# Optimization experiments

Measured on AMD Instinct MI355X. Metric: run time of the kernel, lower is better.

The kernel has to match this reference:

```python
import jax, jax.numpy as jnp
import numpy as np

TAU = 0.7        # init kwarg tau
BIG_NEG = -1.0e9 # matches torch big_neg
B, R = 8192, 4096


def setup_inputs() -> dict:
    key = jax.random.key(0)
    k1, k2 = jax.random.split(key)
    s = jax.random.normal(k1, (B, R), dtype=jnp.float32)
    mask = jax.random.uniform(k2, (B, R), dtype=jnp.float32)  # compared against 0.5
    return {"s": s, "mask": mask, "k": 8}


def reference(s, mask, k):
    # mask-apply then temperature scale
    z = jnp.where(mask > 0.5, s, jnp.full_like(s, BIG_NEG)) / max(TAU, 1e-6)
    # sparsemax along axis 1: sort descending, cumsum, support-size threshold
    z_sorted = -jnp.sort(-z, axis=1)                       # [B, R] descending
    z_cumsum = jnp.cumsum(z_sorted, axis=1)                # [B, R]
    r = jnp.arange(1, R + 1, dtype=z.dtype)[None, :]       # [1, R] ranks 1..R
    cond = 1.0 + r * z_sorted > z_cumsum                   # [B, R] support indicator
    k_sup = jnp.sum(cond, axis=1, keepdims=True)           # [B, 1] int support size
    tau_star = (jnp.take_along_axis(z_cumsum, k_sup - 1, axis=1) - 1.0) / k_sup.astype(z.dtype)
    p = jnp.maximum(z - tau_star, 0.0)                     # sparsemax probs, sum=1
    # scale by budget k and clip to [0, 1]
    return jnp.minimum(jnp.asarray(float(k), z.dtype) * p, 1.0)
```

## Files before the change

kernel.cpp:

```cpp
#include <hip/hip_runtime.h>


#define R_DIM 4096
#define BLOCK 256
#define V4T   4
#define BIG_NEG -1.0e9f
#define INV_TAU (1.0f / 0.7f)

__global__ __launch_bounds__(BLOCK, 6)
void gate_sparsemax_k_kernel(const float* __restrict__ s,
                             const float* __restrict__ m,
                             const int*  __restrict__ kptr,
                             float* __restrict__ out)
{
    __shared__ float red_sum[4];
    __shared__ float red_cnt[4];
    __shared__ float red_max[4];

    const int tid  = (int)threadIdx.x;
    const int lane = tid & 63;
    const int wid  = tid >> 6;
    const int row  = (int)blockIdx.x;

    const float kf = (float)(*kptr);

    const size_t base = (size_t)row * R_DIM;
    const float4* sv4 = (const float4*)(s + base);
    const float4* mv4 = (const float4*)(m + base);
    float4*       ov4 = (float4*)(out + base);

    float4 sv[V4T], mv[V4T];
    #pragma unroll
    for (int t = 0; t < V4T; ++t) sv[t] = sv4[t * BLOCK + tid];
    #pragma unroll
    for (int t = 0; t < V4T; ++t) mv[t] = mv4[t * BLOCK + tid];

    float4 zz[V4T];
    float zmax = -3.4028235e38f;
    #pragma unroll
    for (int t = 0; t < V4T; ++t) {
        float4 zv;
        zv.x = (mv[t].x > 0.5f ? sv[t].x : BIG_NEG) * INV_TAU;
        zv.y = (mv[t].y > 0.5f ? sv[t].y : BIG_NEG) * INV_TAU;
        zv.z = (mv[t].z > 0.5f ? sv[t].z : BIG_NEG) * INV_TAU;
        zv.w = (mv[t].w > 0.5f ? sv[t].w : BIG_NEG) * INV_TAU;
        zz[t] = zv;
        zmax = fmaxf(zmax, fmaxf(fmaxf(zv.x, zv.y), fmaxf(zv.z, zv.w)));
    }

    #pragma unroll
    for (int off = 32; off >= 1; off >>= 1)
        zmax = fmaxf(zmax, __shfl_xor(zmax, off, 64));
    if (lane == 0) red_max[wid] = zmax;
    __syncthreads();
    zmax = fmaxf(fmaxf(red_max[0], red_max[1]), fmaxf(red_max[2], red_max[3]));

    float tau = zmax - 1.0f;
    for (int it = 0; it < 50; ++it) {
        float ssum = 0.0f, cnt = 0.0f;
        #pragma unroll
        for (int t = 0; t < V4T; ++t) {
            const float4 zv = zz[t];
            if (zv.x > tau) { ssum += zv.x; cnt += 1.0f; }
            if (zv.y > tau) { ssum += zv.y; cnt += 1.0f; }
            if (zv.z > tau) { ssum += zv.z; cnt += 1.0f; }
            if (zv.w > tau) { ssum += zv.w; cnt += 1.0f; }
        }
        #pragma unroll
        for (int off = 32; off >= 1; off >>= 1) {
            ssum += __shfl_xor(ssum, off, 64);
            cnt  += __shfl_xor(cnt,  off, 64);
        }
        __syncthreads();
        if (lane == 0) { red_sum[wid] = ssum; red_cnt[wid] = cnt; }
        __syncthreads();
        const float S = ((red_sum[0] + red_sum[1]) + (red_sum[2] + red_sum[3]));
        const float C = ((red_cnt[0] + red_cnt[1]) + (red_cnt[2] + red_cnt[3]));
        const float tnew = (S - 1.0f) / C;
        if (tnew == tau) break;
        tau = tnew;
    }

    #pragma unroll
    for (int t = 0; t < V4T; ++t) {
        const float4 zv = zz[t];
        float4 ov;
        ov.x = fminf(kf * fmaxf(zv.x - tau, 0.0f), 1.0f);
        ov.y = fminf(kf * fmaxf(zv.y - tau, 0.0f), 1.0f);
        ov.z = fminf(kf * fmaxf(zv.z - tau, 0.0f), 1.0f);
        ov.w = fminf(kf * fmaxf(zv.w - tau, 0.0f), 1.0f);
        ov4[t * BLOCK + tid] = ov;
    }
}

extern "C" void kernel_launch(void* const* d_in, const int* in_sizes, int n_in,
                              void* d_out, int out_size, void* d_ws, size_t ws_size,
                              hipStream_t stream) {
    const float* s = (const float*)d_in[0];
    const float* m = (const float*)d_in[1];
    const int*   k = (const int*)d_in[2];
    float* out = (float*)d_out;

    const int nrows = in_sizes[0] / R_DIM;
    gate_sparsemax_k_kernel<<<nrows, BLOCK, 0, stream>>>(s, m, k, out);
}
```

Measured before the change: 312.4 us.

## Use nontemporal loads/stores, double-buffer reduction slots, relax launch bounds

Loads and stores now go through nontemporal builtins so streaming data does not pollute the cache. A scheduling barrier after the loads keeps them issued together. The per-iteration reduction uses ping-pong shared slots, which drops one of the two __syncthreads per bisection iteration. Launch bounds drop from 6 to 4 blocks per CU, which may change register allocation and occupancy.

```diff
diff --git a/kernel.cpp b/kernel.cpp
--- a/kernel.cpp
+++ b/kernel.cpp
@@ -7,14 +7,16 @@
 #define BIG_NEG -1.0e9f
 #define INV_TAU (1.0f / 0.7f)
 
-__global__ __launch_bounds__(BLOCK, 6)
+typedef float fx4 __attribute__((ext_vector_type(4)));
+
+__global__ __launch_bounds__(BLOCK, 4)
 void gate_sparsemax_k_kernel(const float* __restrict__ s,
                              const float* __restrict__ m,
                              const int*  __restrict__ kptr,
                              float* __restrict__ out)
 {
-    __shared__ float red_sum[4];
-    __shared__ float red_cnt[4];
+    __shared__ float red_sum[2][4];
+    __shared__ float red_cnt[2][4];
     __shared__ float red_max[4];
 
     const int tid  = (int)threadIdx.x;
@@ -25,21 +27,22 @@
     const float kf = (float)(*kptr);
 
     const size_t base = (size_t)row * R_DIM;
-    const float4* sv4 = (const float4*)(s + base);
-    const float4* mv4 = (const float4*)(m + base);
-    float4*       ov4 = (float4*)(out + base);
+    const fx4* sv4 = (const fx4*)(s + base);
+    const fx4* mv4 = (const fx4*)(m + base);
+    fx4*       ov4 = (fx4*)(out + base);
 
-    float4 sv[V4T], mv[V4T];
+    fx4 sv[V4T], mv[V4T];
     #pragma unroll
-    for (int t = 0; t < V4T; ++t) sv[t] = sv4[t * BLOCK + tid];
+    for (int t = 0; t < V4T; ++t) sv[t] = __builtin_nontemporal_load(&sv4[t * BLOCK + tid]);
     #pragma unroll
-    for (int t = 0; t < V4T; ++t) mv[t] = mv4[t * BLOCK + tid];
+    for (int t = 0; t < V4T; ++t) mv[t] = __builtin_nontemporal_load(&mv4[t * BLOCK + tid]);
+    __builtin_amdgcn_sched_barrier(0);
 
-    float4 zz[V4T];
+    fx4 zz[V4T];
     float zmax = -3.4028235e38f;
     #pragma unroll
     for (int t = 0; t < V4T; ++t) {
-        float4 zv;
+        fx4 zv;
         zv.x = (mv[t].x > 0.5f ? sv[t].x : BIG_NEG) * INV_TAU;
         zv.y = (mv[t].y > 0.5f ? sv[t].y : BIG_NEG) * INV_TAU;
         zv.z = (mv[t].z > 0.5f ? sv[t].z : BIG_NEG) * INV_TAU;
@@ -60,7 +63,7 @@
         float ssum = 0.0f, cnt = 0.0f;
         #pragma unroll
         for (int t = 0; t < V4T; ++t) {
-            const float4 zv = zz[t];
+            const fx4 zv = zz[t];
             if (zv.x > tau) { ssum += zv.x; cnt += 1.0f; }
             if (zv.y > tau) { ssum += zv.y; cnt += 1.0f; }
             if (zv.z > tau) { ssum += zv.z; cnt += 1.0f; }
@@ -71,11 +74,11 @@
             ssum += __shfl_xor(ssum, off, 64);
             cnt  += __shfl_xor(cnt,  off, 64);
         }
+        const int p = it & 1;
+        if (lane == 0) { red_sum[p][wid] = ssum; red_cnt[p][wid] = cnt; }
         __syncthreads();
-        if (lane == 0) { red_sum[wid] = ssum; red_cnt[wid] = cnt; }
-        __syncthreads();
-        const float S = ((red_sum[0] + red_sum[1]) + (red_sum[2] + red_sum[3]));
-        const float C = ((red_cnt[0] + red_cnt[1]) + (red_cnt[2] + red_cnt[3]));
+        const float S = ((red_sum[p][0] + red_sum[p][1]) + (red_sum[p][2] + red_sum[p][3]));
+        const float C = ((red_cnt[p][0] + red_cnt[p][1]) + (red_cnt[p][2] + red_cnt[p][3]));
         const float tnew = (S - 1.0f) / C;
         if (tnew == tau) break;
         tau = tnew;
@@ -83,13 +86,13 @@
 
     #pragma unroll
     for (int t = 0; t < V4T; ++t) {
-        const float4 zv = zz[t];
-        float4 ov;
+        const fx4 zv = zz[t];
+        fx4 ov;
         ov.x = fminf(kf * fmaxf(zv.x - tau, 0.0f), 1.0f);
         ov.y = fminf(kf * fmaxf(zv.y - tau, 0.0f), 1.0f);
         ov.z = fminf(kf * fmaxf(zv.z - tau, 0.0f), 1.0f);
         ov.w = fminf(kf * fmaxf(zv.w - tau, 0.0f), 1.0f);
-        ov4[t * BLOCK + tid] = ov;
+        __builtin_nontemporal_store(ov, &ov4[t * BLOCK + tid]);
     }
 }
 
```

After: 293.8 us. -6.0%, faster.
